# Performance work log

Hardware: AMD Instinct MI355X
Metric: run time of the kernel (lower is better)

The kernel has to match this reference:

```python
import jax, jax.numpy as jnp
import numpy as np

B, T, D = 2, 2048, 1024
DCD = 4096            # intermediate_dim
RET = 128             # expert_retrieval_dim (split into 2 halves of 64)
NEXP = 4096           # num experts (perfect square)
NKEYS = 64            # sqrt(NEXP)
H = 4                 # n_experts_heads
KPH = 8               # n_experts_per_head


def setup_inputs() -> dict:
    key = jax.random.key(0)
    ks = jax.random.split(key, 10)
    s = lambda k, shape, scale: jax.random.normal(k, shape, jnp.float32) * scale
    return {
        "hidden_states": jax.random.normal(ks[0], (B, T, D), jnp.float32),
        "Wg": s(ks[1], (D, DCD), 0.02), "bg": jnp.zeros((DCD,), jnp.float32),
        "Wu": s(ks[2], (D, DCD), 0.02), "bu": jnp.zeros((DCD,), jnp.float32),
        "Wd": s(ks[3], (DCD, D), 0.02), "bd": jnp.zeros((D,), jnp.float32),
        "Wq": s(ks[4], (D, RET * H), 0.02),          # queries proj (no bias)
        "keys": s(ks[5], (H, NKEYS, 2, RET // 2), 0.02),  # torch inits zeros; randn for a meaningful baseline
        "down_embed": s(ks[6], (NEXP, D), 0.02),
        "up_embed": s(ks[7], (NEXP, D), 0.02),
    }


def reference(hidden_states, Wg, bg, Wu, bu, Wd, bd, Wq, keys, down_embed, up_embed):
    b, t, d = hidden_states.shape
    # product-key retrieval: split query into two halves (p=2)
    q = (hidden_states @ Wq).reshape(b, t, 2, H, RET // 2)
    sim = jnp.einsum('btphn,hkpn->pbthk', q, keys)          # [2,b,t,H,NKEYS]
    sc, ix = jax.lax.top_k(sim, KPH)                        # per-half top-k
    sx, sy = sc[0], sc[1]
    ixx, ixy = ix[0], ix[1]
    all_sc = (sx[..., :, None] + sy[..., None, :]).reshape(b, t, H, KPH * KPH)
    all_ix = (ixx[..., :, None] * NKEYS + ixy[..., None, :]).reshape(b, t, H, KPH * KPH)
    scores, pk = jax.lax.top_k(all_sc, KPH)                 # [b,t,H,KPH]
    idx = jnp.take_along_axis(all_ix, pk, axis=-1)          # expert ids
    de = down_embed[idx]                                    # [b,t,H,KPH,D] gather
    ue = up_embed[idx]                                      # [b,t,H,KPH,D] gather
    w = jnp.einsum('btd,bthkd->bthk', hidden_states, de)
    w = jax.nn.silu(w) * jax.nn.softmax(scores, axis=-1)
    experts_states = jnp.einsum('bthk,bthkd->btd', w, ue)
    mlp = (jax.nn.silu(hidden_states @ Wg + bg) * (hidden_states @ Wu + bu)) @ Wd + bd
    return mlp + experts_states
```

## Files before the change

kernel.cpp:

```cpp
#include <hip/hip_runtime.h>
#include <hip/hip_bf16.h>
#include <stdint.h>

typedef unsigned short u16;
typedef __attribute__((ext_vector_type(8))) short short8;
typedef __attribute__((ext_vector_type(4))) float f32x4;

union B8 { short8 v; u16 u[8]; };
union U4 { unsigned long long q; u16 u[4]; };

__device__ __forceinline__ float b2f(u16 b) {
  union { unsigned int i; float f; } x; x.i = ((unsigned int)b) << 16; return x.f;
}
__device__ __forceinline__ u16 f2b(float f) {
  __hip_bfloat16 h = __float2bfloat16(f);
  return *reinterpret_cast<u16*>(&h);
}

#define GLOAD_LDS16(gp, lp)                                                  \
  __builtin_amdgcn_global_load_lds(                                          \
      (const __attribute__((address_space(1))) unsigned int*)(gp),           \
      (__attribute__((address_space(3))) unsigned int*)(lp), 16, 0, 0)

__global__ __launch_bounds__(256) void cvt_f2b(const float* __restrict__ src,
                                               u16* __restrict__ dst) {
  size_t i = ((size_t)blockIdx.x * 256 + threadIdx.x) * 4;
  f32x4 v = *(const f32x4*)(src + i);
  U4 o;
#pragma unroll
  for (int j = 0; j < 4; ++j) o.u[j] = f2b(v[j]);
  *(unsigned long long*)(dst + i) = o.q;
}

__global__ __launch_bounds__(256) void convt_w(const float* __restrict__ W,
                                               u16* __restrict__ WT,
                                               int K, int N) {
  int k  = blockIdx.x * 64 + (threadIdx.x & 63);
  int n8 = blockIdx.y * 32 + (threadIdx.x >> 6) * 8;
  const float* p = W + (size_t)k * N + n8;
  f32x4 a = *(const f32x4*)(p);
  f32x4 b = *(const f32x4*)(p + 4);
#pragma unroll
  for (int j = 0; j < 4; ++j) WT[(size_t)(n8 + j) * K + k] = f2b(a[j]);
#pragma unroll
  for (int j = 0; j < 4; ++j) WT[(size_t)(n8 + 4 + j) * K + k] = f2b(b[j]);
}

__global__ __launch_bounds__(256) void convt_keys(const float* __restrict__ keys,
                                                  float* __restrict__ keysT) {
  int h = blockIdx.x, p = blockIdx.y;
  int k  = threadIdx.x >> 2;
  int n0 = (threadIdx.x & 3) * 16;
  const float* src = keys + ((size_t)(h * 64 + k) * 2 + p) * 64 + n0;
  float* dst = keysT + (((size_t)h * 2 + p) * 64) * 64 + k;
#pragma unroll
  for (int c = 0; c < 16; ++c)
    dst[(size_t)(n0 + c) * 64] = src[c];
}

__global__ __launch_bounds__(256) void gemm_bf16(
    const u16* __restrict__ A, const u16* __restrict__ BT,
    const float* __restrict__ bias,
    u16* __restrict__ Cb, int M, int N, int K)
{
  __shared__ __attribute__((aligned(16))) u16 As[128 * 32];
  __shared__ __attribute__((aligned(16))) u16 Bs[128 * 32];
  int tid = threadIdx.x;
  int m0 = blockIdx.y * 128, n0 = blockIdx.x * 128;
  int wave = tid >> 6, lane = tid & 63;
  int wm = (wave >> 1) * 64, wn = (wave & 1) * 64;
  int quad = lane >> 4, r16 = lane & 15;
  int seg0 = wave * 2, seg1 = wave * 2 + 1;
  int srow = lane >> 2, scol = (lane & 3) * 8;

  const u16* a0 = A  + (size_t)(m0 + seg0 * 16 + srow) * K + scol;
  const u16* a1 = A  + (size_t)(m0 + seg1 * 16 + srow) * K + scol;
  const u16* b0 = BT + (size_t)(n0 + seg0 * 16 + srow) * K + scol;
  const u16* b1 = BT + (size_t)(n0 + seg1 * 16 + srow) * K + scol;

  f32x4 acc[4][4] = {};

  for (int k0 = 0; k0 < K; k0 += 32) {
    GLOAD_LDS16(a0 + k0, As + seg0 * 512);
    GLOAD_LDS16(a1 + k0, As + seg1 * 512);
    GLOAD_LDS16(b0 + k0, Bs + seg0 * 512);
    GLOAD_LDS16(b1 + k0, Bs + seg1 * 512);
    __syncthreads();
    short8 af[4], bfr[4];
#pragma unroll
    for (int i = 0; i < 4; ++i)
      af[i] = *(const short8*)(&As[(wm + i * 16 + r16) * 32 + quad * 8]);
#pragma unroll
    for (int j = 0; j < 4; ++j)
      bfr[j] = *(const short8*)(&Bs[(wn + j * 16 + r16) * 32 + quad * 8]);
#pragma unroll
    for (int i = 0; i < 4; ++i)
#pragma unroll
      for (int j = 0; j < 4; ++j)
        acc[i][j] = __builtin_amdgcn_mfma_f32_16x16x32_bf16(af[i], bfr[j], acc[i][j], 0, 0, 0);
    __syncthreads();
  }

#pragma unroll
  for (int i = 0; i < 4; ++i) {
    int row = m0 + wm + i * 16 + quad * 4;
#pragma unroll
    for (int j = 0; j < 4; ++j) {
      int col = n0 + wn + j * 16 + r16;
      float bv = bias ? bias[col] : 0.f;
#pragma unroll
      for (int r = 0; r < 4; ++r) {
        float v = acc[i][j][r] + bv;
        Cb[(size_t)(row + r) * N + col] = f2b(v);
      }
    }
  }
}

__global__ __launch_bounds__(256) void gemm_dsk(
    const u16* __restrict__ A, const u16* __restrict__ BT,
    float* __restrict__ P, int M, int N, int K, int Kslice, int mOff)
{
  __shared__ __attribute__((aligned(16))) u16 As[128 * 32];
  __shared__ __attribute__((aligned(16))) u16 Bs[128 * 32];
  int tid = threadIdx.x;
  int m0 = blockIdx.y * 128, n0 = blockIdx.x * 128;
  int kb = blockIdx.z * Kslice, ke = kb + Kslice;
  int wave = tid >> 6, lane = tid & 63;
  int wm = (wave >> 1) * 64, wn = (wave & 1) * 64;
  int quad = lane >> 4, r16 = lane & 15;
  int seg0 = wave * 2, seg1 = wave * 2 + 1;
  int srow = lane >> 2, scol = (lane & 3) * 8;

  const u16* a0 = A  + (size_t)(m0 + seg0 * 16 + srow) * K + scol;
  const u16* a1 = A  + (size_t)(m0 + seg1 * 16 + srow) * K + scol;
  const u16* b0 = BT + (size_t)(n0 + seg0 * 16 + srow) * K + scol;
  const u16* b1 = BT + (size_t)(n0 + seg1 * 16 + srow) * K + scol;

  f32x4 acc[4][4] = {};

  for (int k0 = kb; k0 < ke; k0 += 32) {
    GLOAD_LDS16(a0 + k0, As + seg0 * 512);
    GLOAD_LDS16(a1 + k0, As + seg1 * 512);
    GLOAD_LDS16(b0 + k0, Bs + seg0 * 512);
    GLOAD_LDS16(b1 + k0, Bs + seg1 * 512);
    __syncthreads();
    short8 af[4], bfr[4];
#pragma unroll
    for (int i = 0; i < 4; ++i)
      af[i] = *(const short8*)(&As[(wm + i * 16 + r16) * 32 + quad * 8]);
#pragma unroll
    for (int j = 0; j < 4; ++j)
      bfr[j] = *(const short8*)(&Bs[(wn + j * 16 + r16) * 32 + quad * 8]);
#pragma unroll
    for (int i = 0; i < 4; ++i)
#pragma unroll
      for (int j = 0; j < 4; ++j)
        acc[i][j] = __builtin_amdgcn_mfma_f32_16x16x32_bf16(af[i], bfr[j], acc[i][j], 0, 0, 0);
    __syncthreads();
  }

  float* Pz = P + (size_t)blockIdx.z * 4194304;
#pragma unroll
  for (int i = 0; i < 4; ++i) {
    int row = mOff + m0 + wm + i * 16 + quad * 4;
#pragma unroll
    for (int j = 0; j < 4; ++j) {
      int col = n0 + wn + j * 16 + r16;
#pragma unroll
      for (int r = 0; r < 4; ++r)
        Pz[(size_t)(row + r) * N + col] = acc[i][j][r];
    }
  }
}

__global__ __launch_bounds__(256) void reduce_k(const float* __restrict__ part,
                                                int S,
                                                const float* __restrict__ es,
                                                const float* __restrict__ bd,
                                                float* __restrict__ out) {
  int t = blockIdx.x, c0 = threadIdx.x * 4;
  size_t off = (size_t)t * 1024 + c0;
  f32x4 a = *(const f32x4*)(es + off);
  for (int s = 0; s < S; ++s) {
    f32x4 p = *(const f32x4*)(part + (size_t)s * 4194304 + off);
#pragma unroll
    for (int c = 0; c < 4; ++c) a[c] += p[c];
  }
  f32x4 b = *(const f32x4*)(bd + c0);
  f32x4 o;
#pragma unroll
  for (int c = 0; c < 4; ++c) o[c] = a[c] + b[c];
  *(f32x4*)(out + off) = o;
}

__global__ __launch_bounds__(256, 2) void gemm_gu(
    const u16* __restrict__ A, const u16* __restrict__ BgT,
    const u16* __restrict__ BuT,
    const float* __restrict__ bg, const float* __restrict__ bu,
    u16* __restrict__ H, int M, int N, int K)
{
  __shared__ __attribute__((aligned(16))) u16 As[128 * 32];
  __shared__ __attribute__((aligned(16))) u16 Gs[128 * 32];
  __shared__ __attribute__((aligned(16))) u16 Us[128 * 32];
  int tid = threadIdx.x;
  int m0 = blockIdx.y * 128, n0 = blockIdx.x * 128;
  int wave = tid >> 6, lane = tid & 63;
  int wm = (wave >> 1) * 64, wn = (wave & 1) * 64;
  int quad = lane >> 4, r16 = lane & 15;
  int seg0 = wave * 2, seg1 = wave * 2 + 1;
  int srow = lane >> 2, scol = (lane & 3) * 8;

  const u16* a0 = A   + (size_t)(m0 + seg0 * 16 + srow) * K + scol;
  const u16* a1 = A   + (size_t)(m0 + seg1 * 16 + srow) * K + scol;
  const u16* g0 = BgT + (size_t)(n0 + seg0 * 16 + srow) * K + scol;
  const u16* g1 = BgT + (size_t)(n0 + seg1 * 16 + srow) * K + scol;
  const u16* u0 = BuT + (size_t)(n0 + seg0 * 16 + srow) * K + scol;
  const u16* u1 = BuT + (size_t)(n0 + seg1 * 16 + srow) * K + scol;

  f32x4 ag[4][4] = {}, au[4][4] = {};

  for (int k0 = 0; k0 < K; k0 += 32) {
    GLOAD_LDS16(a0 + k0, As + seg0 * 512);
    GLOAD_LDS16(a1 + k0, As + seg1 * 512);
    GLOAD_LDS16(g0 + k0, Gs + seg0 * 512);
    GLOAD_LDS16(g1 + k0, Gs + seg1 * 512);
    GLOAD_LDS16(u0 + k0, Us + seg0 * 512);
    GLOAD_LDS16(u1 + k0, Us + seg1 * 512);
    __syncthreads();
    short8 af[4], bfr[4];
#pragma unroll
    for (int i = 0; i < 4; ++i)
      af[i] = *(const short8*)(&As[(wm + i * 16 + r16) * 32 + quad * 8]);
#pragma unroll
    for (int j = 0; j < 4; ++j)
      bfr[j] = *(const short8*)(&Gs[(wn + j * 16 + r16) * 32 + quad * 8]);
#pragma unroll
    for (int i = 0; i < 4; ++i)
#pragma unroll
      for (int j = 0; j < 4; ++j)
        ag[i][j] = __builtin_amdgcn_mfma_f32_16x16x32_bf16(af[i], bfr[j], ag[i][j], 0, 0, 0);
#pragma unroll
    for (int j = 0; j < 4; ++j)
      bfr[j] = *(const short8*)(&Us[(wn + j * 16 + r16) * 32 + quad * 8]);
#pragma unroll
    for (int i = 0; i < 4; ++i)
#pragma unroll
      for (int j = 0; j < 4; ++j)
        au[i][j] = __builtin_amdgcn_mfma_f32_16x16x32_bf16(af[i], bfr[j], au[i][j], 0, 0, 0);
    __syncthreads();
  }

#pragma unroll
  for (int i = 0; i < 4; ++i) {
    int row = m0 + wm + i * 16 + quad * 4;
#pragma unroll
    for (int j = 0; j < 4; ++j) {
      int col = n0 + wn + j * 16 + r16;
      float bgv = bg[col], buv = bu[col];
#pragma unroll
      for (int r = 0; r < 4; ++r) {
        float g = ag[i][j][r] + bgv;
        float u = au[i][j][r] + buv;
        float h = (g / (1.f + __expf(-g))) * u;
        H[(size_t)(row + r) * N + col] = f2b(h);
      }
    }
  }
}

template<int NP>
__device__ __forceinline__ void sort8_desc(float (&v)[NP], int (&ii)[NP], int j) {
#pragma unroll
  for (int k = 2; k <= 8; k <<= 1) {
#pragma unroll
    for (int s = k >> 1; s > 0; s >>= 1) {
      bool desc  = (j & k) == 0;
      bool lower = (j & s) == 0;
#pragma unroll
      for (int p = 0; p < NP; ++p) {
        float vp = __shfl_xor(v[p], s);
        int   ip = __shfl_xor(ii[p], s);
        bool mf = (v[p] > vp) || (v[p] == vp && ii[p] < ip);
        bool keep = (desc == lower) ? mf : !mf;
        if (!keep) { v[p] = vp; ii[p] = ip; }
      }
    }
  }
}

template<int NP>
__device__ __forceinline__ void merge_top8(float (&v)[NP], int (&ii)[NP], int j) {
#pragma unroll
  for (int r = 0; r < 3; ++r) {
    int mask = (8 << r) | 7;
#pragma unroll
    for (int p = 0; p < NP; ++p) {
      float vp = __shfl_xor(v[p], mask);
      int   ip = __shfl_xor(ii[p], mask);
      bool mf = (v[p] > vp) || (v[p] == vp && ii[p] < ip);
      if (!mf) { v[p] = vp; ii[p] = ip; }
    }
#pragma unroll
    for (int s = 4; s > 0; s >>= 1) {
      bool lower = (j & s) == 0;
#pragma unroll
      for (int p = 0; p < NP; ++p) {
        float vq = __shfl_xor(v[p], s);
        int   iq = __shfl_xor(ii[p], s);
        bool mf = (v[p] > vq) || (v[p] == vq && ii[p] < iq);
        bool keep = lower ? mf : !mf;
        if (!keep) { v[p] = vq; ii[p] = iq; }
      }
    }
  }
}

__global__ __launch_bounds__(256) void retrieve_k(
    const u16*  __restrict__ q,
    const float* __restrict__ keysT,
    int* __restrict__ idx_out,
    float* __restrict__ p_out)
{
  int t = blockIdx.x;
  int w = threadIdx.x >> 6, lane = threadIdx.x & 63;
  int j = lane & 7;

  float v[2]; int ii[2];
#pragma unroll
  for (int p = 0; p < 2; ++p) {
    const u16*   qp = q + (size_t)t * 512 + p * 256 + w * 64;
    const float* kp = keysT + ((size_t)(w * 2 + p) * 64) * 64 + lane;
    float s0 = 0.f, s1 = 0.f, s2 = 0.f, s3 = 0.f;
#pragma unroll
    for (int n = 0; n < 64; n += 8) {
      B8 qv; qv.v = *(const short8*)(qp + n);
      s0 += b2f(qv.u[0]) * kp[(size_t)(n + 0) * 64];
      s1 += b2f(qv.u[1]) * kp[(size_t)(n + 1) * 64];
      s2 += b2f(qv.u[2]) * kp[(size_t)(n + 2) * 64];
      s3 += b2f(qv.u[3]) * kp[(size_t)(n + 3) * 64];
      s0 += b2f(qv.u[4]) * kp[(size_t)(n + 4) * 64];
      s1 += b2f(qv.u[5]) * kp[(size_t)(n + 5) * 64];
      s2 += b2f(qv.u[6]) * kp[(size_t)(n + 6) * 64];
      s3 += b2f(qv.u[7]) * kp[(size_t)(n + 7) * 64];
    }
    v[p] = (s0 + s1) + (s2 + s3); ii[p] = lane;
  }

  sort8_desc<2>(v, ii, j);
  merge_top8<2>(v, ii, j);

  float v2[1] = { __shfl(v[0], lane >> 3) + __shfl(v[1], lane & 7) };
  int  pos[1] = { lane };
  merge_top8<1>(v2, pos, j);

  int ex = __shfl(ii[0], pos[0] >> 3);
  int ey = __shfl(ii[1], pos[0] & 7);

  float m = __shfl(v2[0], 0);
  float e = __expf(v2[0] - m);
  float sum = e;
#pragma unroll
  for (int s = 4; s > 0; s >>= 1) sum += __shfl_xor(sum, s);

  if (lane < 8) {
    int o = (t * 4 + w) * 8 + lane;
    p_out[o]   = e / sum;
    idx_out[o] = ex * 64 + ey;
  }
}

__global__ __launch_bounds__(256) void expert_k(
    const u16* __restrict__ xb, const u16* __restrict__ downb,
    const u16* __restrict__ upb,
    const int* __restrict__ idx, const float* __restrict__ probs,
    float* __restrict__ es)
{
  __shared__ float acc_s[4][1024];
  int t = blockIdx.x;
  int w = threadIdx.x >> 6, lane = threadIdx.x & 63;
  const size_t tb = (size_t)t * 1024;
  const int lo = lane * 8;

  B8 xv0, xv1;
  xv0.v = *(const short8*)(xb + tb + lo);
  xv1.v = *(const short8*)(xb + tb + 512 + lo);
  float xf[16];
#pragma unroll
  for (int c = 0; c < 8; ++c) { xf[c] = b2f(xv0.u[c]); xf[8 + c] = b2f(xv1.u[c]); }

  float a[16] = {};
#pragma unroll
  for (int e8 = 0; e8 < 8; ++e8) {
    int e = w * 8 + e8;
    int id = idx[t * 32 + e];
    const u16* dp = downb + (size_t)id * 1024;
    B8 d0, d1;
    d0.v = *(const short8*)(dp + lo);
    d1.v = *(const short8*)(dp + 512 + lo);
    float part = 0.f;
#pragma unroll
    for (int c = 0; c < 8; ++c)
      part += xf[c] * b2f(d0.u[c]) + xf[8 + c] * b2f(d1.u[c]);
#pragma unroll
    for (int off = 32; off; off >>= 1) part += __shfl_xor(part, off);
    float gate = (part / (1.f + __expf(-part))) * probs[t * 32 + e];
    const u16* upp = upb + (size_t)id * 1024;
    B8 u0, u1;
    u0.v = *(const short8*)(upp + lo);
    u1.v = *(const short8*)(upp + 512 + lo);
#pragma unroll
    for (int c = 0; c < 8; ++c) {
      a[c]     += gate * b2f(u0.u[c]);
      a[8 + c] += gate * b2f(u1.u[c]);
    }
  }
#pragma unroll
  for (int c = 0; c < 8; ++c) {
    acc_s[w][lo + c]       = a[c];
    acc_s[w][512 + lo + c] = a[8 + c];
  }
  __syncthreads();
  int d0i = threadIdx.x * 4;
  f32x4 s0 = *(const f32x4*)(&acc_s[0][d0i]);
  f32x4 s1 = *(const f32x4*)(&acc_s[1][d0i]);
  f32x4 s2 = *(const f32x4*)(&acc_s[2][d0i]);
  f32x4 s3 = *(const f32x4*)(&acc_s[3][d0i]);
  f32x4 o;
#pragma unroll
  for (int c = 0; c < 4; ++c) o[c] = (s0[c] + s1[c]) + (s2[c] + s3[c]);
  *(f32x4*)(es + tb + d0i) = o;
}

extern "C" void kernel_launch(void* const* d_in, const int* in_sizes, int n_in,
                              void* d_out, int out_size, void* d_ws, size_t ws_size,
                              hipStream_t stream)
{
  const float* x    = (const float*)d_in[0];
  const float* Wg   = (const float*)d_in[1];
  const float* bg   = (const float*)d_in[2];
  const float* Wu   = (const float*)d_in[3];
  const float* bu   = (const float*)d_in[4];
  const float* Wd   = (const float*)d_in[5];
  const float* bd   = (const float*)d_in[6];
  const float* Wq   = (const float*)d_in[7];
  const float* keys = (const float*)d_in[8];
  const float* down = (const float*)d_in[9];
  const float* up   = (const float*)d_in[10];
  float* out = (float*)d_out;

  const size_t MB = 1048576;
  char* ws = (char*)d_ws;
  u16*   xb    = (u16*)(ws);
  u16*   WgT   = (u16*)(ws + 8  * MB);
  u16*   WuT   = (u16*)(ws + 16 * MB);
  u16*   WdT   = (u16*)(ws + 24 * MB);
  float* es    = (float*)(ws + 32 * MB);
  u16*   WqT   = (u16*)(ws + 32 * MB);
  u16*   qb    = (u16*)(ws + 34 * MB);
  float* keysT = (float*)(ws + 47 * MB);
  int*   idxb  = (int*)(ws + 48 * MB);
  float* prb   = (float*)(ws + 48 * MB + 512 * 1024);
  u16*   downb = (u16*)(ws + 49 * MB);
  u16*   upb   = (u16*)(ws + 57 * MB);

  int S = 4;
  while (S > 1 && 65 * MB + (size_t)S * 16 * MB + 1 * MB > ws_size) S >>= 1;
  float* part = (float*)(ws + 65 * MB);
  size_t gboff = 65 * MB + (size_t)S * 16 * MB;
  u16*   gb    = (u16*)(ws + gboff);

  size_t avail = ws_size > gboff ? ws_size - gboff : 0;
  int rows = 4096;
  while (rows > 128 && (size_t)rows * 4096 * 2 > avail) rows >>= 1;
  int Ksl = 4096 / S;

  cvt_f2b<<<4096, 256, 0, stream>>>(x, xb);
  cvt_f2b<<<4096, 256, 0, stream>>>(down, downb);
  cvt_f2b<<<4096, 256, 0, stream>>>(up, upb);
  convt_w<<<dim3(16, 16),  256, 0, stream>>>(Wq, WqT, 1024, 512);
  convt_w<<<dim3(16, 128), 256, 0, stream>>>(Wg, WgT, 1024, 4096);
  convt_w<<<dim3(16, 128), 256, 0, stream>>>(Wu, WuT, 1024, 4096);
  convt_w<<<dim3(64, 32),  256, 0, stream>>>(Wd, WdT, 4096, 1024);
  convt_keys<<<dim3(4, 2), 256, 0, stream>>>(keys, keysT);

  gemm_bf16<<<dim3(4, 32), 256, 0, stream>>>(xb, WqT, nullptr,
                                             qb, 4096, 512, 1024);
  retrieve_k<<<4096, 256, 0, stream>>>(qb, keysT, idxb, prb);
  expert_k<<<4096, 256, 0, stream>>>(xb, downb, upb, idxb, prb, es);

  for (int m0c = 0; m0c < 4096; m0c += rows) {
    int gy = rows / 128;
    gemm_gu<<<dim3(32, gy), 256, 0, stream>>>(xb + (size_t)m0c * 1024, WgT, WuT,
                                              bg, bu, gb, rows, 4096, 1024);
    gemm_dsk<<<dim3(8, gy, S), 256, 0, stream>>>(gb, WdT, part,
                                                 rows, 1024, 4096, Ksl, m0c);
  }
  reduce_k<<<4096, 256, 0, stream>>>(part, S, es, bd, out);
}
```

Baseline: 455.7 us.

## Replace fused gate/up GEMM with double-buffered 256x256 tile GEMM run twice

```diff
diff --git a/kernel.cpp b/kernel.cpp
--- a/kernel.cpp
+++ b/kernel.cpp
@@ -117,6 +117,112 @@
   }
 }
 
+__global__ __launch_bounds__(512, 2) void g9(
+    const u16* __restrict__ A, const u16* __restrict__ BT,
+    const float* __restrict__ bias, const u16* __restrict__ U,
+    u16* __restrict__ C, int N, int K, int mode)
+{
+  __shared__ __attribute__((aligned(16))) u16 lds[65536];
+  int lid = blockIdx.y * gridDim.x + blockIdx.x;
+  int cpx = (gridDim.x * gridDim.y) >> 3;
+  int swz = (lid & 7) * cpx + (lid >> 3);
+  int bx = swz % gridDim.x, by = swz / gridDim.x;
+
+  int tid = threadIdx.x;
+  int m0 = by * 256, n0 = bx * 256;
+  int wid = tid >> 6, l = tid & 63;
+  int wm = wid >> 2, wn = wid & 3;
+  int quad = l >> 4, r16 = l & 15;
+  int NT = K >> 6;
+  int xsw = (r16 & 7) << 3;
+
+  int srow = wid * 8 + (l >> 3);
+  int sblk = (l & 7) ^ (l >> 3);
+  const u16* Ag = A  + (size_t)(m0 + srow) * K + sblk * 8;
+  const u16* Bg = BT + (size_t)(n0 + srow) * K + sblk * 8;
+
+#define STG_A(tt, h) do { u16* d_ = lds + (((tt) & 1) << 14) + (h) * 8192 + wid * 512;         \
+  GLOAD_LDS16(Ag + (size_t)((h) * 128) * K + (size_t)(tt) * 64, d_);                           \
+  GLOAD_LDS16(Ag + (size_t)((h) * 128 + 64) * K + (size_t)(tt) * 64, d_ + 4096); } while (0)
+#define STG_B(tt, h) do { u16* d_ = lds + 32768 + (((tt) & 1) << 14) + (h) * 8192 + wid * 512; \
+  GLOAD_LDS16(Bg + (size_t)((h) * 128) * K + (size_t)(tt) * 64, d_);                           \
+  GLOAD_LDS16(Bg + (size_t)((h) * 128 + 64) * K + (size_t)(tt) * 64, d_ + 4096); } while (0)
+
+  f32x4 acc[8][4] = {};
+
+  STG_B(0, 0); STG_B(0, 1); STG_A(0, 0); STG_A(0, 1);
+
+  for (int t = 0; t < NT; ++t) {
+    const u16* La = lds + ((t & 1) << 14);
+    const u16* Lb = La + 32768;
+    bool more = (t + 1 < NT);
+    short8 bfr[4][2];
+#pragma unroll
+    for (int q = 0; q < 4; ++q) {
+      if (q == 0) {
+        if (more) { STG_B(t + 1, 0); asm volatile("s_waitcnt vmcnt(2)" ::: "memory"); }
+        else      { asm volatile("s_waitcnt vmcnt(0)" ::: "memory"); }
+        __builtin_amdgcn_s_barrier();
+      } else if (q == 1) { if (more) STG_B(t + 1, 1); }
+      else if (q == 2)   { if (more) STG_A(t + 1, 0); }
+      else               { if (more) STG_A(t + 1, 1); }
+
+      if (q == 0) {
+#pragma unroll
+        for (int nf = 0; nf < 4; ++nf)
+#pragma unroll
+          for (int sk = 0; sk < 2; ++sk)
+            bfr[nf][sk] = *(const short8*)(Lb + (wn * 64 + nf * 16 + r16) * 64
+                                           + ((sk * 32 + quad * 8) ^ xsw));
+      }
+      short8 af[2][2];
+#pragma unroll
+      for (int i = 0; i < 2; ++i)
+#pragma unroll
+        for (int sk = 0; sk < 2; ++sk)
+          af[i][sk] = *(const short8*)(La + (wm * 128 + (q * 2 + i) * 16 + r16) * 64
+                                       + ((sk * 32 + quad * 8) ^ xsw));
+      asm volatile("s_waitcnt lgkmcnt(0)" ::: "memory");
+      __builtin_amdgcn_sched_barrier(0);
+      __builtin_amdgcn_s_setprio(1);
+#pragma unroll
+      for (int i = 0; i < 2; ++i)
+#pragma unroll
+        for (int nf = 0; nf < 4; ++nf)
+#pragma unroll
+          for (int sk = 0; sk < 2; ++sk)
+            acc[q * 2 + i][nf] = __builtin_amdgcn_mfma_f32_16x16x32_bf16(
+                af[i][sk], bfr[nf][sk], acc[q * 2 + i][nf], 0, 0, 0);
+      __builtin_amdgcn_s_setprio(0);
+    }
+    __builtin_amdgcn_s_barrier();
+  }
+#undef STG_A
+#undef STG_B
+
+#pragma unroll
+  for (int mf = 0; mf < 8; ++mf) {
+#pragma unroll
+    for (int nf = 0; nf < 4; ++nf) {
+      int col = n0 + wn * 64 + nf * 16 + r16;
+      float bv = bias[col];
+#pragma unroll
+      for (int r = 0; r < 4; ++r) {
+        int row = m0 + wm * 128 + mf * 16 + quad * 4 + r;
+        float g = acc[mf][nf][r] + bv;
+        float h;
+        if (mode == 1) {
+          float u = b2f(U[(size_t)row * N + col]);
+          h = (g / (1.f + __expf(-g))) * u;
+        } else {
+          h = g;
+        }
+        C[(size_t)row * N + col] = f2b(h);
+      }
+    }
+  }
+}
+
 __global__ __launch_bounds__(256) void gemm_dsk(
     const u16* __restrict__ A, const u16* __restrict__ BT,
     float* __restrict__ P, int M, int N, int K, int Kslice, int mOff)
@@ -192,81 +298,6 @@
 #pragma unroll
   for (int c = 0; c < 4; ++c) o[c] = a[c] + b[c];
   *(f32x4*)(out + off) = o;
-}
-
-__global__ __launch_bounds__(256, 2) void gemm_gu(
-    const u16* __restrict__ A, const u16* __restrict__ BgT,
-    const u16* __restrict__ BuT,
-    const float* __restrict__ bg, const float* __restrict__ bu,
-    u16* __restrict__ H, int M, int N, int K)
-{
-  __shared__ __attribute__((aligned(16))) u16 As[128 * 32];
-  __shared__ __attribute__((aligned(16))) u16 Gs[128 * 32];
-  __shared__ __attribute__((aligned(16))) u16 Us[128 * 32];
-  int tid = threadIdx.x;
-  int m0 = blockIdx.y * 128, n0 = blockIdx.x * 128;
-  int wave = tid >> 6, lane = tid & 63;
-  int wm = (wave >> 1) * 64, wn = (wave & 1) * 64;
-  int quad = lane >> 4, r16 = lane & 15;
-  int seg0 = wave * 2, seg1 = wave * 2 + 1;
-  int srow = lane >> 2, scol = (lane & 3) * 8;
-
-  const u16* a0 = A   + (size_t)(m0 + seg0 * 16 + srow) * K + scol;
-  const u16* a1 = A   + (size_t)(m0 + seg1 * 16 + srow) * K + scol;
-  const u16* g0 = BgT + (size_t)(n0 + seg0 * 16 + srow) * K + scol;
-  const u16* g1 = BgT + (size_t)(n0 + seg1 * 16 + srow) * K + scol;
-  const u16* u0 = BuT + (size_t)(n0 + seg0 * 16 + srow) * K + scol;
-  const u16* u1 = BuT + (size_t)(n0 + seg1 * 16 + srow) * K + scol;
-
-  f32x4 ag[4][4] = {}, au[4][4] = {};
-
-  for (int k0 = 0; k0 < K; k0 += 32) {
-    GLOAD_LDS16(a0 + k0, As + seg0 * 512);
-    GLOAD_LDS16(a1 + k0, As + seg1 * 512);
-    GLOAD_LDS16(g0 + k0, Gs + seg0 * 512);
-    GLOAD_LDS16(g1 + k0, Gs + seg1 * 512);
-    GLOAD_LDS16(u0 + k0, Us + seg0 * 512);
-    GLOAD_LDS16(u1 + k0, Us + seg1 * 512);
-    __syncthreads();
-    short8 af[4], bfr[4];
-#pragma unroll
-    for (int i = 0; i < 4; ++i)
-      af[i] = *(const short8*)(&As[(wm + i * 16 + r16) * 32 + quad * 8]);
-#pragma unroll
-    for (int j = 0; j < 4; ++j)
-      bfr[j] = *(const short8*)(&Gs[(wn + j * 16 + r16) * 32 + quad * 8]);
-#pragma unroll
-    for (int i = 0; i < 4; ++i)
-#pragma unroll
-      for (int j = 0; j < 4; ++j)
-        ag[i][j] = __builtin_amdgcn_mfma_f32_16x16x32_bf16(af[i], bfr[j], ag[i][j], 0, 0, 0);
-#pragma unroll
-    for (int j = 0; j < 4; ++j)
-      bfr[j] = *(const short8*)(&Us[(wn + j * 16 + r16) * 32 + quad * 8]);
-#pragma unroll
-    for (int i = 0; i < 4; ++i)
-#pragma unroll
-      for (int j = 0; j < 4; ++j)
-        au[i][j] = __builtin_amdgcn_mfma_f32_16x16x32_bf16(af[i], bfr[j], au[i][j], 0, 0, 0);
-    __syncthreads();
-  }
-
-#pragma unroll
-  for (int i = 0; i < 4; ++i) {
-    int row = m0 + wm + i * 16 + quad * 4;
-#pragma unroll
-    for (int j = 0; j < 4; ++j) {
-      int col = n0 + wn + j * 16 + r16;
-      float bgv = bg[col], buv = bu[col];
-#pragma unroll
-      for (int r = 0; r < 4; ++r) {
-        float g = ag[i][j][r] + bgv;
-        float u = au[i][j][r] + buv;
-        float h = (g / (1.f + __expf(-g))) * u;
-        H[(size_t)(row + r) * N + col] = f2b(h);
-      }
-    }
-  }
 }
 
 template<int NP>
@@ -463,17 +494,10 @@
   float* prb   = (float*)(ws + 48 * MB + 512 * 1024);
   u16*   downb = (u16*)(ws + 49 * MB);
   u16*   upb   = (u16*)(ws + 57 * MB);
-
-  int S = 4;
-  while (S > 1 && 65 * MB + (size_t)S * 16 * MB + 1 * MB > ws_size) S >>= 1;
-  float* part = (float*)(ws + 65 * MB);
-  size_t gboff = 65 * MB + (size_t)S * 16 * MB;
-  u16*   gb    = (u16*)(ws + gboff);
-
-  size_t avail = ws_size > gboff ? ws_size - gboff : 0;
-  int rows = 4096;
-  while (rows > 128 && (size_t)rows * 4096 * 2 > avail) rows >>= 1;
-  int Ksl = 4096 / S;
+  float* part  = (float*)(ws + 65 * MB);
+  u16*   Ub    = (u16*)(ws + 65 * MB);
+  u16*   gb    = (u16*)(ws + 129 * MB);
+  const int S = 4;
 
   cvt_f2b<<<4096, 256, 0, stream>>>(x, xb);
   cvt_f2b<<<4096, 256, 0, stream>>>(down, downb);
@@ -489,12 +513,9 @@
   retrieve_k<<<4096, 256, 0, stream>>>(qb, keysT, idxb, prb);
   expert_k<<<4096, 256, 0, stream>>>(xb, downb, upb, idxb, prb, es);
 
-  for (int m0c = 0; m0c < 4096; m0c += rows) {
-    int gy = rows / 128;
-    gemm_gu<<<dim3(32, gy), 256, 0, stream>>>(xb + (size_t)m0c * 1024, WgT, WuT,
-                                              bg, bu, gb, rows, 4096, 1024);
-    gemm_dsk<<<dim3(8, gy, S), 256, 0, stream>>>(gb, WdT, part,
-                                                 rows, 1024, 4096, Ksl, m0c);
-  }
+  g9<<<dim3(16, 16), 512, 0, stream>>>(xb, WuT, bu, nullptr, Ub, 4096, 1024, 0);
+  g9<<<dim3(16, 16), 512, 0, stream>>>(xb, WgT, bg, Ub, gb, 4096, 1024, 1);
+  gemm_dsk<<<dim3(8, 32, S), 256, 0, stream>>>(gb, WdT, part,
+                                               4096, 1024, 4096, 4096 / S, 0);
   reduce_k<<<4096, 256, 0, stream>>>(part, S, es, bd, out);
 }
```

New measurement: 471.1 us. 3.4% more time.
